# Performance work log

Measured on AMD Instinct MI355X. Metric: run time of the kernel, lower is better.

Reference implementation:

```python
import jax, jax.numpy as jnp
import numpy as np

EMBED_DIM = 400          # d; entity embedding is 2d (alpha|beta)
N_ENTITY = 100000
N_RELATION = 500
HIDDEN = 1600
BATCH = 8192


def _reg(x):
    # Regularizer(base_add=1, min_val=0.05, max_val=1e9)
    return jnp.clip(x + 1.0, 0.05, 1e9)


def setup_inputs() -> dict:
    key = jax.random.key(0)
    ks = jax.random.split(key, 16)
    d = EMBED_DIM
    rng = (9.0 + 2.0) / d  # (gamma + epsilon) / embed_dim with gamma=9

    def xavier(k, shape):
        fan_out, fan_in = shape
        lim = np.sqrt(6.0 / (fan_in + fan_out))
        return jax.random.uniform(k, shape, jnp.float32, -lim, lim)

    inp = {
        "anchor1_idx": jax.random.randint(ks[0], (BATCH,), 0, N_ENTITY),
        "rel1_idx": jax.random.randint(ks[1], (BATCH,), 0, N_RELATION),
        "anchor2_idx": jax.random.randint(ks[2], (BATCH,), 0, N_ENTITY),
        "rel2_idx": jax.random.randint(ks[3], (BATCH,), 0, N_RELATION),
        # embedding tables
        "entity_embedding": jax.random.uniform(ks[4], (N_ENTITY, 2 * d), jnp.float32, -rng, rng),
        "relation_embedding": jax.random.uniform(ks[5], (N_RELATION, d), jnp.float32, -rng, rng),
        # BetaProjection: layer1 [hidden, 2d+d], layer2 [hidden, hidden], layer0 [2d, hidden]
        "pW1": xavier(ks[6], (HIDDEN, 3 * d)),
        "pb1": jnp.zeros((HIDDEN,), jnp.float32),
        "pW2": xavier(ks[7], (HIDDEN, HIDDEN)),
        "pb2": jnp.zeros((HIDDEN,), jnp.float32),
        "pW0": xavier(ks[8], (2 * d, HIDDEN)),
        "pb0": jnp.zeros((2 * d,), jnp.float32),
        # BetaIntersection: layer1 [2d, 2d], layer2 [d, 2d]
        "iW1": xavier(ks[9], (2 * d, 2 * d)),
        "ib1": jnp.zeros((2 * d,), jnp.float32),
        "iW2": xavier(ks[10], (d, 2 * d)),
        "ib2": jnp.zeros((d,), jnp.float32),
    }
    return inp


def _projection(e_emb, r_emb, pW1, pb1, pW2, pb2, pW0, pb0):
    # cat -> Linear+ReLU (layer1) -> Linear+ReLU (layer2) -> layer0 -> regularizer
    x = jnp.concatenate([e_emb, r_emb], axis=-1)           # [B, 3d]
    x = jax.nn.relu(x @ pW1.T + pb1)                       # [B, H]
    x = jax.nn.relu(x @ pW2.T + pb2)                       # [B, H]
    x = x @ pW0.T + pb0                                    # [B, 2d]
    return _reg(x)


def _intersection(alphas, betas, iW1, ib1, iW2, ib2):
    # alphas/betas: [K, B, d]; softmax attention over K
    all_emb = jnp.concatenate([alphas, betas], axis=-1)    # [K, B, 2d]
    h = jax.nn.relu(all_emb @ iW1.T + ib1)                 # [K, B, 2d]
    att = jax.nn.softmax(h @ iW2.T + ib2, axis=0)          # [K, B, d]
    return jnp.sum(att * alphas, axis=0), jnp.sum(att * betas, axis=0)


def reference(anchor1_idx, rel1_idx, anchor2_idx, rel2_idx,
              entity_embedding, relation_embedding,
              pW1, pb1, pW2, pb2, pW0, pb0,
              iW1, ib1, iW2, ib2):
    h = _reg(entity_embedding)                             # entity_regularizer
    r = relation_embedding

    emb1 = _projection(h[anchor1_idx], r[rel1_idx], pW1, pb1, pW2, pb2, pW0, pb0)
    a1, b1 = jnp.split(emb1, 2, axis=-1)
    emb2 = _projection(h[anchor2_idx], r[rel2_idx], pW1, pb1, pW2, pb2, pW0, pb0)
    a2, b2 = jnp.split(emb2, 2, axis=-1)

    alpha, beta = _intersection(jnp.stack([a1, a2]), jnp.stack([b1, b2]),
                                iW1, ib1, iW2, ib2)
    return alpha, beta
```

## Files before the change

### kernel.cpp

```cpp
#include <hip/hip_runtime.h>
#include <hip/hip_bf16.h>
#include <stdint.h>

typedef __bf16 bf16_t;
typedef __bf16 bf16x8 __attribute__((ext_vector_type(8)));
typedef float f32x4 __attribute__((ext_vector_type(4)));

constexpr int BATCH = 8192;
constexpr int M = 2 * BATCH;

constexpr int K1 = 1216;
constexpr int N1c = 1792;
constexpr int LDC1 = 1664, NS1 = 1600;
constexpr int LDA2 = 1664, KL2 = 1600;
constexpr int N2c = 1792;
constexpr int LDC2 = 1664, NS2 = 1600;
constexpr int LDA3 = 1664, KL3 = 1600;
constexpr int N3c = 1024;
constexpr int LDC3 = 1024, NS3 = 832;
constexpr int LDA4 = 1024, KL4 = 832;
constexpr int N4c = 1024;
constexpr int LDC4 = 1024, NS4 = 832;
constexpr int LDA5 = 1024, KL5 = 832, N5 = 512;

__device__ __forceinline__ void gload_lds16(const void* g, void* l) {
  __builtin_amdgcn_global_load_lds(
      (const __attribute__((address_space(1))) void*)g,
      (__attribute__((address_space(3))) void*)l,
      16, 0, 0);
}

#define CFENCE() asm volatile("" ::: "memory")
#define BAR()  { CFENCE(); __builtin_amdgcn_s_barrier(); CFENCE(); }

__device__ __forceinline__ void doconv(int idx, const float* __restrict__ src,
                                       bf16_t* __restrict__ dst, int Nr, int Kc, int Kp) {
  const int kp4 = Kp >> 2;
  const int r = idx / kp4;
  const int c = (idx - r * kp4) << 2;
  union { bf16_t h[4]; uint2 u; } pk;
#pragma unroll
  for (int j = 0; j < 4; ++j) {
    const int cc = c + j;
    const float v = (r < Nr && cc < Kc) ? src[(size_t)r * Kc + cc] : 0.f;
    pk.h[j] = (bf16_t)v;
  }
  *(uint2*)(dst + (size_t)r * Kp + c) = pk.u;
}

constexpr int CJ0 = N1c * K1 / 4;
constexpr int CJ1 = CJ0 + N2c * LDA2 / 4;
constexpr int CJ2 = CJ1 + N3c * LDA3 / 4;
constexpr int CJ3 = CJ2 + N4c * LDA4 / 4;
constexpr int CJ4 = CJ3 + N5 * LDA5 / 4;
constexpr int CONV_BLOCKS = CJ4 / 256;
constexpr int PREP_BLOCKS = M + CONV_BLOCKS;

__global__ void prep_kernel(const int* __restrict__ a1, const int* __restrict__ r1,
                            const int* __restrict__ a2, const int* __restrict__ r2,
                            const float* __restrict__ ent, const float* __restrict__ rel,
                            bf16_t* __restrict__ X,
                            const float* __restrict__ pW1, const float* __restrict__ pW2,
                            const float* __restrict__ pW0, const float* __restrict__ iW1,
                            const float* __restrict__ iW2,
                            bf16_t* __restrict__ W1b, bf16_t* __restrict__ W2b,
                            bf16_t* __restrict__ W0b, bf16_t* __restrict__ iW1b,
                            bf16_t* __restrict__ iW2b) {
  if (blockIdx.x < M) {
    const int row = blockIdx.x;
    const int b   = row & (BATCH - 1);
    const int br  = row >> 13;
    const int eidx = br ? a2[b] : a1[b];
    const int ridx = br ? r2[b] : r1[b];
    const float* __restrict__ esrc = ent + (size_t)eidx * 800;
    const float* __restrict__ rsrc = rel + (size_t)ridx * 400;
    bf16_t* __restrict__ dst = X + (size_t)row * K1;
    for (int g = threadIdx.x; g < K1 / 4; g += 256) {
      const int c = g * 4;
      float4 v = make_float4(0.f, 0.f, 0.f, 0.f);
      if (c < 800) {
        v = *(const float4*)(esrc + c);
        v.x = fminf(fmaxf(v.x + 1.f, 0.05f), 1e9f);
        v.y = fminf(fmaxf(v.y + 1.f, 0.05f), 1e9f);
        v.z = fminf(fmaxf(v.z + 1.f, 0.05f), 1e9f);
        v.w = fminf(fmaxf(v.w + 1.f, 0.05f), 1e9f);
      } else if (c < 1200) {
        v = *(const float4*)(rsrc + (c - 800));
      }
      union { bf16_t h[4]; uint2 u; } pk;
      pk.h[0] = (bf16_t)v.x; pk.h[1] = (bf16_t)v.y;
      pk.h[2] = (bf16_t)v.z; pk.h[3] = (bf16_t)v.w;
      *(uint2*)(dst + c) = pk.u;
    }
  } else {
    const int idx = (blockIdx.x - M) * 256 + threadIdx.x;
    if (idx < CJ0)      doconv(idx,        pW1, W1b, 1600, 1200, K1);
    else if (idx < CJ1) doconv(idx - CJ0,  pW2, W2b, 1600, 1600, LDA2);
    else if (idx < CJ2) doconv(idx - CJ1,  pW0, W0b,  800, 1600, LDA3);
    else if (idx < CJ3) doconv(idx - CJ2,  iW1, iW1b, 800,  800, LDA4);
    else if (idx < CJ4) doconv(idx - CJ3,  iW2, iW2b, 400,  800, LDA5);
  }
}

enum { ACT_RELU = 0, ACT_REG = 1 };

template <int ACT>
__global__ __launch_bounds__(512)
void gemm256(const bf16_t* __restrict__ A, const bf16_t* __restrict__ Bw,
             const float* __restrict__ bias, int Nbias,
             bf16_t* __restrict__ Cb,
             int lda, int Nstore, int ldc, int NT, int gridN) {
  __shared__ __align__(16) bf16_t lds[8][8192];

  const int nwg = gridDim.x;
  const int id = blockIdx.x;
  const int swz = (id & 7) * (nwg >> 3) + (id >> 3);
  const int bn = swz % gridN, bm = swz / gridN;

  const int t = threadIdx.x;
  const int lane = t & 63;
  const int wv = t >> 6;
  const int wm = wv >> 2, wn = wv & 3;
  const int l15 = lane & 15;
  const int kbs = (((lane >> 4) ^ ((l15 >> 1) & 3)) << 4);

  const int srow = t >> 2;
  const int skc  = (t & 3) ^ ((t >> 3) & 3);
  const bf16_t* aR0 = A  + (size_t)(bm * 256 + srow) * lda + skc * 8;
  const bf16_t* aR1 = aR0 + (size_t)128 * lda;
  const bf16_t* bR0 = Bw + (size_t)(bn * 256 + srow) * lda + skc * 8;
  const bf16_t* bR1 = bR0 + (size_t)128 * lda;
  const int ldsb0 = (wv * 64) * 16;
  const int ldsb1 = (512 + wv * 64) * 16;

  auto STAGE = [&](const bf16_t* r0p, const bf16_t* r1p, int kOff, bf16_t* slot) {
    gload_lds16(r0p + kOff, (char*)slot + ldsb0);
    gload_lds16(r1p + kOff, (char*)slot + ldsb1);
  };

  f32x4 acc[8][4];
#pragma unroll
  for (int i = 0; i < 8; ++i)
#pragma unroll
    for (int j = 0; j < 4; ++j) acc[i][j] = f32x4{0.f, 0.f, 0.f, 0.f};

  STAGE(aR0, aR1, 0, lds[0]);
  STAGE(bR0, bR1, 0, lds[2]);
  STAGE(aR0, aR1, 32, lds[1]);
  STAGE(bR0, bR1, 32, lds[3]);
  if (NT > 1) {
    STAGE(aR0, aR1, 64, lds[4]);
    STAGE(bR0, bR1, 64, lds[6]);
    asm volatile("s_waitcnt vmcnt(8)" ::: "memory");
  } else {
    asm volatile("s_waitcnt vmcnt(4)" ::: "memory");
  }
  __builtin_amdgcn_s_barrier();
  CFENCE();

  bf16x8 bfr[4];
  int db = 0;
  for (int kt = 0; kt < NT; ++kt, db ^= 1) {
    const bool p1 = (kt + 1) < NT;
    const bool p2 = (kt + 2) < NT;
    bf16_t* const cur = (bf16_t*)lds[db * 4];
    bf16_t* const nxt = (bf16_t*)lds[(db ^ 1) * 4];

    {
      const char* sA = (const char*)(cur);
      const char* sB = (const char*)(cur + 2 * 8192);
      bf16x8 af[4];
#pragma unroll
      for (int i = 0; i < 4; ++i)
        af[i] = *(const bf16x8*)(sA + ((wm * 128 + i * 16 + l15) << 6) + kbs);
#pragma unroll
      for (int i = 0; i < 4; ++i)
        bfr[i] = *(const bf16x8*)(sB + ((wn * 64 + i * 16 + l15) << 6) + kbs);
      if (p1) STAGE(aR0, aR1, (kt + 1) * 64 + 32, nxt + 1 * 8192);
      BAR();
      __builtin_amdgcn_s_setprio(1);
#pragma unroll
      for (int i = 0; i < 4; ++i)
#pragma unroll
        for (int j = 0; j < 4; ++j)
          acc[i][j] = __builtin_amdgcn_mfma_f32_16x16x32_bf16(af[i], bfr[j], acc[i][j], 0, 0, 0);
      __builtin_amdgcn_s_setprio(0);
      BAR();
    }
    {
      const char* sA = (const char*)(cur);
      bf16x8 af[4];
#pragma unroll
      for (int i = 0; i < 4; ++i)
        af[i] = *(const bf16x8*)(sA + ((wm * 128 + (4 + i) * 16 + l15) << 6) + kbs);
      if (p1) STAGE(bR0, bR1, (kt + 1) * 64 + 32, nxt + 3 * 8192);
      BAR();
      __builtin_amdgcn_s_setprio(1);
#pragma unroll
      for (int i = 0; i < 4; ++i)
#pragma unroll
        for (int j = 0; j < 4; ++j)
          acc[4 + i][j] = __builtin_amdgcn_mfma_f32_16x16x32_bf16(af[i], bfr[j], acc[4 + i][j], 0, 0, 0);
      __builtin_amdgcn_s_setprio(0);
      if (p1) asm volatile("s_waitcnt vmcnt(8)" ::: "memory");
      else    asm volatile("s_waitcnt vmcnt(0)" ::: "memory");
      BAR();
    }
    {
      const char* sA = (const char*)(cur + 1 * 8192);
      const char* sB = (const char*)(cur + 3 * 8192);
      bf16x8 af[4];
#pragma unroll
      for (int i = 0; i < 4; ++i)
        af[i] = *(const bf16x8*)(sA + ((wm * 128 + i * 16 + l15) << 6) + kbs);
#pragma unroll
      for (int i = 0; i < 4; ++i)
        bfr[i] = *(const bf16x8*)(sB + ((wn * 64 + i * 16 + l15) << 6) + kbs);
      if (p2) STAGE(aR0, aR1, (kt + 2) * 64, cur + 0 * 8192);
      BAR();
      __builtin_amdgcn_s_setprio(1);
#pragma unroll
      for (int i = 0; i < 4; ++i)
#pragma unroll
        for (int j = 0; j < 4; ++j)
          acc[i][j] = __builtin_amdgcn_mfma_f32_16x16x32_bf16(af[i], bfr[j], acc[i][j], 0, 0, 0);
      __builtin_amdgcn_s_setprio(0);
      BAR();
    }
    {
      const char* sA = (const char*)(cur + 1 * 8192);
      bf16x8 af[4];
#pragma unroll
      for (int i = 0; i < 4; ++i)
        af[i] = *(const bf16x8*)(sA + ((wm * 128 + (4 + i) * 16 + l15) << 6) + kbs);
      if (p2) STAGE(bR0, bR1, (kt + 2) * 64, cur + 2 * 8192);
      BAR();
      __builtin_amdgcn_s_setprio(1);
#pragma unroll
      for (int i = 0; i < 4; ++i)
#pragma unroll
        for (int j = 0; j < 4; ++j)
          acc[4 + i][j] = __builtin_amdgcn_mfma_f32_16x16x32_bf16(af[i], bfr[j], acc[4 + i][j], 0, 0, 0);
      __builtin_amdgcn_s_setprio(0);
      if (p1) {
        if (p2) asm volatile("s_waitcnt vmcnt(8)" ::: "memory");
        else    asm volatile("s_waitcnt vmcnt(4)" ::: "memory");
      }
      BAR();
    }
  }

  const int r0 = bm * 256 + wm * 128 + ((lane >> 4) * 4);
  const int c0 = bn * 256 + wn * 64 + l15;
#pragma unroll
  for (int ni = 0; ni < 4; ++ni) {
    const int col = c0 + ni * 16;
    const float bv = (col < Nbias) ? bias[col] : 0.f;
    const bool cok = (col < Nstore);
#pragma unroll
    for (int mi = 0; mi < 8; ++mi) {
#pragma unroll
      for (int j = 0; j < 4; ++j) {
        float v = acc[mi][ni][j] + bv;
        if (ACT == ACT_RELU) v = fmaxf(v, 0.f);
        else                 v = fminf(fmaxf(v + 1.f, 0.05f), 1e9f);
        if (cok) Cb[(size_t)(r0 + mi * 16 + j) * ldc + col] = (bf16_t)v;
      }
    }
  }
}

__global__ __launch_bounds__(256)
void g5_combine(const bf16_t* __restrict__ H, const bf16_t* __restrict__ Wb,
                const float* __restrict__ ib2, const bf16_t* __restrict__ E,
                float* __restrict__ out) {
  __shared__ __align__(16) bf16_t As1[128 * 64];
  __shared__ __align__(16) bf16_t As2[128 * 64];
  __shared__ __align__(16) bf16_t Bs[128 * 64];

  const int bn = blockIdx.x, bm = blockIdx.y;
  const int t = threadIdx.x;
  const int lane = t & 63;
  const int wv = t >> 6;
  const int wm = wv >> 1, wn = wv & 1;

  f32x4 acc1[4][4], acc2[4][4];
#pragma unroll
  for (int i = 0; i < 4; ++i)
#pragma unroll
    for (int j = 0; j < 4; ++j) { acc1[i][j] = f32x4{0.f,0.f,0.f,0.f}; acc2[i][j] = f32x4{0.f,0.f,0.f,0.f}; }

  const size_t a1Base = (size_t)(bm * 128) * LDA5;
  const size_t a2Base = (size_t)(8192 + bm * 128) * LDA5;
  const size_t bBase  = (size_t)(bn * 128) * LDA5;

  for (int kt = 0; kt < KL5; kt += 64) {
    __syncthreads();
#pragma unroll
    for (int q = 0; q < 4; ++q) {
      const int lin = q * 256 + t;
      const int row = lin >> 3;
      const int kc = ((lin & 7) ^ (row & 7)) * 8;
      const int lofs = (q * 256 + wv * 64) * 16;
      gload_lds16(H + a1Base + (size_t)row * LDA5 + kt + kc, (char*)As1 + lofs);
      gload_lds16(H + a2Base + (size_t)row * LDA5 + kt + kc, (char*)As2 + lofs);
      gload_lds16(Wb + bBase + (size_t)row * LDA5 + kt + kc, (char*)Bs + lofs);
    }
    __syncthreads();

#pragma unroll
    for (int s = 0; s < 2; ++s) {
      const int crd = s * 4 + (lane >> 4);
      const int k0 = (crd ^ (lane & 7)) * 8;
      bf16x8 af1[4], af2[4], bf[4];
#pragma unroll
      for (int i = 0; i < 4; ++i) {
        const int ra = wm * 64 + i * 16 + (lane & 15);
        af1[i] = *(const bf16x8*)(As1 + ra * 64 + k0);
        af2[i] = *(const bf16x8*)(As2 + ra * 64 + k0);
        const int rb = wn * 64 + i * 16 + (lane & 15);
        bf[i] = *(const bf16x8*)(Bs + rb * 64 + k0);
      }
#pragma unroll
      for (int mi = 0; mi < 4; ++mi)
#pragma unroll
        for (int ni = 0; ni < 4; ++ni) {
          acc1[mi][ni] = __builtin_amdgcn_mfma_f32_16x16x32_bf16(af1[mi], bf[ni], acc1[mi][ni], 0, 0, 0);
          acc2[mi][ni] = __builtin_amdgcn_mfma_f32_16x16x32_bf16(af2[mi], bf[ni], acc2[mi][ni], 0, 0, 0);
        }
    }
  }

  const int rloc0 = wm * 64 + ((lane >> 4) * 4);
  const int cloc0 = wn * 64 + (lane & 15);
#pragma unroll
  for (int ni = 0; ni < 4; ++ni) {
    const int d = bn * 128 + cloc0 + ni * 16;
    if (d >= 400) continue;
    const float bv = ib2[d];
#pragma unroll
    for (int mi = 0; mi < 4; ++mi) {
#pragma unroll
      for (int j = 0; j < 4; ++j) {
        const int b = bm * 128 + rloc0 + mi * 16 + j;
        const float l1 = acc1[mi][ni][j] + bv;
        const float l2 = acc2[mi][ni][j] + bv;
        const float att1 = 1.f / (1.f + expf(l2 - l1));
        const float att2 = 1.f - att1;
        const bf16_t* E1 = E + (size_t)b * LDC3;
        const bf16_t* E2 = E + (size_t)(8192 + b) * LDC3;
        out[(size_t)b * 400 + d] =
            att1 * (float)E1[d] + att2 * (float)E2[d];
        out[(size_t)8192 * 400 + (size_t)b * 400 + d] =
            att1 * (float)E1[400 + d] + att2 * (float)E2[400 + d];
      }
    }
  }
}

extern "C" void kernel_launch(void* const* d_in, const int* in_sizes, int n_in,
                              void* d_out, int out_size, void* d_ws, size_t ws_size,
                              hipStream_t stream) {
  const int* a1 = (const int*)d_in[0];
  const int* r1 = (const int*)d_in[1];
  const int* a2 = (const int*)d_in[2];
  const int* r2 = (const int*)d_in[3];
  const float* ent = (const float*)d_in[4];
  const float* rel = (const float*)d_in[5];
  const float* pW1 = (const float*)d_in[6];
  const float* pb1 = (const float*)d_in[7];
  const float* pW2 = (const float*)d_in[8];
  const float* pb2 = (const float*)d_in[9];
  const float* pW0 = (const float*)d_in[10];
  const float* pb0 = (const float*)d_in[11];
  const float* iW1 = (const float*)d_in[12];
  const float* ib1 = (const float*)d_in[13];
  const float* iW2 = (const float*)d_in[14];
  const float* ib2 = (const float*)d_in[15];

  char* ws = (char*)d_ws;
  size_t o = 0;
  auto take = [&](size_t bytes) { char* p = ws + o; o += (bytes + 255) & ~(size_t)255; return p; };
  bf16_t* W1b  = (bf16_t*)take((size_t)N1c * K1 * 2);
  bf16_t* W2b  = (bf16_t*)take((size_t)N2c * LDA2 * 2);
  bf16_t* W0b  = (bf16_t*)take((size_t)N3c * LDA3 * 2);
  bf16_t* iW1b = (bf16_t*)take((size_t)N4c * LDA4 * 2);
  bf16_t* iW2b = (bf16_t*)take((size_t)N5 * LDA5 * 2);
  char* bufX = take((size_t)M * K1 * 2);
  char* bufY = take((size_t)M * LDC1 * 2);
  char* bufZ = take((size_t)M * LDC2 * 2);

  bf16_t* Xb = (bf16_t*)bufX;
  bf16_t* Yb = (bf16_t*)bufY;
  bf16_t* Zb = (bf16_t*)bufZ;
  bf16_t* Eb = (bf16_t*)bufX;
  bf16_t* Hb = (bf16_t*)bufY;

  prep_kernel<<<dim3(PREP_BLOCKS), 256, 0, stream>>>(a1, r1, a2, r2, ent, rel, Xb,
                                                     pW1, pW2, pW0, iW1, iW2,
                                                     W1b, W2b, W0b, iW1b, iW2b);

  gemm256<ACT_RELU><<<dim3((N1c / 256) * (M / 256)), 512, 0, stream>>>(
      Xb, W1b, pb1, 1600, Yb, K1, NS1, LDC1, K1 / 64, N1c / 256);
  gemm256<ACT_RELU><<<dim3((N2c / 256) * (M / 256)), 512, 0, stream>>>(
      Yb, W2b, pb2, 1600, Zb, LDA2, NS2, LDC2, KL2 / 64, N2c / 256);
  gemm256<ACT_REG><<<dim3((N3c / 256) * (M / 256)), 512, 0, stream>>>(
      Zb, W0b, pb0, 800, Eb, LDA3, NS3, LDC3, KL3 / 64, N3c / 256);
  gemm256<ACT_RELU><<<dim3((N4c / 256) * (M / 256)), 512, 0, stream>>>(
      Eb, iW1b, ib1, 800, Hb, LDA4, NS4, LDC4, KL4 / 64, N4c / 256);
  g5_combine<<<dim3(N5 / 128, BATCH / 128), 256, 0, stream>>>(
      Hb, iW2b, ib2, Eb, (float*)d_out);
}
```

Measured before the change: 348.7 us.

## Use mixed 192/256-wide N tiles for hidden GEMMs, double-buffer g5, grid-stride prep

```diff
diff --git a/kernel.cpp b/kernel.cpp
--- a/kernel.cpp
+++ b/kernel.cpp
@@ -10,10 +10,8 @@
 constexpr int M = 2 * BATCH;
 
 constexpr int K1 = 1216;
-constexpr int N1c = 1792;
 constexpr int LDC1 = 1664, NS1 = 1600;
 constexpr int LDA2 = 1664, KL2 = 1600;
-constexpr int N2c = 1792;
 constexpr int LDC2 = 1664, NS2 = 1600;
 constexpr int LDA3 = 1664, KL3 = 1600;
 constexpr int N3c = 1024;
@@ -22,6 +20,7 @@
 constexpr int N4c = 1024;
 constexpr int LDC4 = 1024, NS4 = 832;
 constexpr int LDA5 = 1024, KL5 = 832, N5 = 512;
+constexpr int NW1 = 1792, NW2 = 1792;
 
 __device__ __forceinline__ void gload_lds16(const void* g, void* l) {
   __builtin_amdgcn_global_load_lds(
@@ -48,13 +47,14 @@
   *(uint2*)(dst + (size_t)r * Kp + c) = pk.u;
 }
 
-constexpr int CJ0 = N1c * K1 / 4;
-constexpr int CJ1 = CJ0 + N2c * LDA2 / 4;
+constexpr int CJ0 = NW1 * K1 / 4;
+constexpr int CJ1 = CJ0 + NW2 * LDA2 / 4;
 constexpr int CJ2 = CJ1 + N3c * LDA3 / 4;
 constexpr int CJ3 = CJ2 + N4c * LDA4 / 4;
 constexpr int CJ4 = CJ3 + N5 * LDA5 / 4;
-constexpr int CONV_BLOCKS = CJ4 / 256;
-constexpr int PREP_BLOCKS = M + CONV_BLOCKS;
+constexpr int GATHERB = 2048;
+constexpr int CONVB = 2048;
+constexpr int PREPB = GATHERB + CONVB;
 
 __global__ void prep_kernel(const int* __restrict__ a1, const int* __restrict__ r1,
                             const int* __restrict__ a2, const int* __restrict__ r2,
@@ -66,217 +66,238 @@
                             bf16_t* __restrict__ W1b, bf16_t* __restrict__ W2b,
                             bf16_t* __restrict__ W0b, bf16_t* __restrict__ iW1b,
                             bf16_t* __restrict__ iW2b) {
-  if (blockIdx.x < M) {
-    const int row = blockIdx.x;
-    const int b   = row & (BATCH - 1);
-    const int br  = row >> 13;
-    const int eidx = br ? a2[b] : a1[b];
-    const int ridx = br ? r2[b] : r1[b];
-    const float* __restrict__ esrc = ent + (size_t)eidx * 800;
-    const float* __restrict__ rsrc = rel + (size_t)ridx * 400;
-    bf16_t* __restrict__ dst = X + (size_t)row * K1;
-    for (int g = threadIdx.x; g < K1 / 4; g += 256) {
-      const int c = g * 4;
-      float4 v = make_float4(0.f, 0.f, 0.f, 0.f);
-      if (c < 800) {
-        v = *(const float4*)(esrc + c);
-        v.x = fminf(fmaxf(v.x + 1.f, 0.05f), 1e9f);
-        v.y = fminf(fmaxf(v.y + 1.f, 0.05f), 1e9f);
-        v.z = fminf(fmaxf(v.z + 1.f, 0.05f), 1e9f);
-        v.w = fminf(fmaxf(v.w + 1.f, 0.05f), 1e9f);
-      } else if (c < 1200) {
-        v = *(const float4*)(rsrc + (c - 800));
+  if (blockIdx.x < GATHERB) {
+    for (int r8 = 0; r8 < 8; ++r8) {
+      const int row = blockIdx.x * 8 + r8;
+      const int b   = row & (BATCH - 1);
+      const int br  = row >> 13;
+      const int eidx = br ? a2[b] : a1[b];
+      const int ridx = br ? r2[b] : r1[b];
+      const float* __restrict__ esrc = ent + (size_t)eidx * 800;
+      const float* __restrict__ rsrc = rel + (size_t)ridx * 400;
+      bf16_t* __restrict__ dst = X + (size_t)row * K1;
+      for (int g = threadIdx.x; g < K1 / 4; g += 256) {
+        const int c = g * 4;
+        float4 v = make_float4(0.f, 0.f, 0.f, 0.f);
+        if (c < 800) {
+          v = *(const float4*)(esrc + c);
+          v.x = fminf(fmaxf(v.x + 1.f, 0.05f), 1e9f);
+          v.y = fminf(fmaxf(v.y + 1.f, 0.05f), 1e9f);
+          v.z = fminf(fmaxf(v.z + 1.f, 0.05f), 1e9f);
+          v.w = fminf(fmaxf(v.w + 1.f, 0.05f), 1e9f);
+        } else if (c < 1200) {
+          v = *(const float4*)(rsrc + (c - 800));
+        }
+        union { bf16_t h[4]; uint2 u; } pk;
+        pk.h[0] = (bf16_t)v.x; pk.h[1] = (bf16_t)v.y;
+        pk.h[2] = (bf16_t)v.z; pk.h[3] = (bf16_t)v.w;
+        *(uint2*)(dst + c) = pk.u;
       }
-      union { bf16_t h[4]; uint2 u; } pk;
-      pk.h[0] = (bf16_t)v.x; pk.h[1] = (bf16_t)v.y;
-      pk.h[2] = (bf16_t)v.z; pk.h[3] = (bf16_t)v.w;
-      *(uint2*)(dst + c) = pk.u;
     }
   } else {
-    const int idx = (blockIdx.x - M) * 256 + threadIdx.x;
-    if (idx < CJ0)      doconv(idx,        pW1, W1b, 1600, 1200, K1);
-    else if (idx < CJ1) doconv(idx - CJ0,  pW2, W2b, 1600, 1600, LDA2);
-    else if (idx < CJ2) doconv(idx - CJ1,  pW0, W0b,  800, 1600, LDA3);
-    else if (idx < CJ3) doconv(idx - CJ2,  iW1, iW1b, 800,  800, LDA4);
-    else if (idx < CJ4) doconv(idx - CJ3,  iW2, iW2b, 400,  800, LDA5);
+    for (int idx = (blockIdx.x - GATHERB) * 256 + threadIdx.x; idx < CJ4;
+         idx += CONVB * 256) {
+      if (idx < CJ0)      doconv(idx,        pW1, W1b, 1600, 1200, K1);
+      else if (idx < CJ1) doconv(idx - CJ0,  pW2, W2b, 1600, 1600, LDA2);
+      else if (idx < CJ2) doconv(idx - CJ1,  pW0, W0b,  800, 1600, LDA3);
+      else if (idx < CJ3) doconv(idx - CJ2,  iW1, iW1b, 800,  800, LDA4);
+      else                doconv(idx - CJ3,  iW2, iW2b, 400,  800, LDA5);
+    }
   }
 }
 
 enum { ACT_RELU = 0, ACT_REG = 1 };
 
-template <int ACT>
+template <int ACT, int NFR>
+__device__ __forceinline__
+void gemm_body(const bf16_t* __restrict__ A, const bf16_t* __restrict__ Bw,
+               const float* __restrict__ bias, int Nbias, bf16_t* __restrict__ Cb,
+               int lda, int Nstore, int ldc, int NT, int bm, int col0,
+               bf16_t* ldsbase, int t) {
+  const int lane = t & 63;
+  const int wv = t >> 6;
+  const int wm = wv >> 2, wn = wv & 3;
+  const int l15 = lane & 15;
+  const int kbs = (((lane >> 4) ^ ((l15 >> 1) & 3)) << 4);
+
+  const int srow = t >> 2;
+  const int skc  = (t & 3) ^ ((t >> 3) & 3);
+  const bf16_t* aR0 = A  + (size_t)(bm * 256 + srow) * lda + skc * 8;
+  const bf16_t* aR1 = aR0 + (size_t)128 * lda;
+  const bf16_t* bR0 = Bw + (size_t)(col0 + srow) * lda + skc * 8;
+  const bf16_t* bR1 = bR0 + (size_t)128 * lda;
+  const int ldsb0 = (wv * 64) * 16;
+  const int ldsb1 = (512 + wv * 64) * 16;
+
+  auto SLOT = [&](int s) { return ldsbase + s * 8192; };
+  auto STAGE = [&](const bf16_t* r0p, const bf16_t* r1p, int kOff, bf16_t* slot) {
+    gload_lds16(r0p + kOff, (char*)slot + ldsb0);
+    gload_lds16(r1p + kOff, (char*)slot + ldsb1);
+  };
+
+  f32x4 acc[8][NFR];
+#pragma unroll
+  for (int i = 0; i < 8; ++i)
+#pragma unroll
+    for (int j = 0; j < NFR; ++j) acc[i][j] = f32x4{0.f, 0.f, 0.f, 0.f};
+
+  STAGE(aR0, aR1, 0, SLOT(0));
+  STAGE(bR0, bR1, 0, SLOT(2));
+  STAGE(aR0, aR1, 32, SLOT(1));
+  STAGE(bR0, bR1, 32, SLOT(3));
+  if (NT > 1) {
+    STAGE(aR0, aR1, 64, SLOT(4));
+    STAGE(bR0, bR1, 64, SLOT(6));
+    asm volatile("s_waitcnt vmcnt(8)" ::: "memory");
+  } else {
+    asm volatile("s_waitcnt vmcnt(4)" ::: "memory");
+  }
+  __builtin_amdgcn_s_barrier();
+  CFENCE();
+
+  bf16x8 bfr[NFR];
+  int db = 0;
+  for (int kt = 0; kt < NT; ++kt, db ^= 1) {
+    const bool p1 = (kt + 1) < NT;
+    const bool p2 = (kt + 2) < NT;
+    bf16_t* const cur = SLOT(db * 4);
+    bf16_t* const nxt = SLOT((db ^ 1) * 4);
+
+    {
+      const char* sA = (const char*)(cur);
+      const char* sB = (const char*)(cur + 2 * 8192);
+      bf16x8 af[4];
+#pragma unroll
+      for (int i = 0; i < 4; ++i)
+        af[i] = *(const bf16x8*)(sA + ((wm * 128 + i * 16 + l15) << 6) + kbs);
+#pragma unroll
+      for (int i = 0; i < NFR; ++i)
+        bfr[i] = *(const bf16x8*)(sB + ((wn * (NFR * 16) + i * 16 + l15) << 6) + kbs);
+      if (p1) STAGE(aR0, aR1, (kt + 1) * 64 + 32, nxt + 1 * 8192);
+      BAR();
+      __builtin_amdgcn_s_setprio(1);
+#pragma unroll
+      for (int i = 0; i < 4; ++i)
+#pragma unroll
+        for (int j = 0; j < NFR; ++j)
+          acc[i][j] = __builtin_amdgcn_mfma_f32_16x16x32_bf16(af[i], bfr[j], acc[i][j], 0, 0, 0);
+      __builtin_amdgcn_s_setprio(0);
+      BAR();
+    }
+    {
+      const char* sA = (const char*)(cur);
+      bf16x8 af[4];
+#pragma unroll
+      for (int i = 0; i < 4; ++i)
+        af[i] = *(const bf16x8*)(sA + ((wm * 128 + (4 + i) * 16 + l15) << 6) + kbs);
+      if (p1) STAGE(bR0, bR1, (kt + 1) * 64 + 32, nxt + 3 * 8192);
+      BAR();
+      __builtin_amdgcn_s_setprio(1);
+#pragma unroll
+      for (int i = 0; i < 4; ++i)
+#pragma unroll
+        for (int j = 0; j < NFR; ++j)
+          acc[4 + i][j] = __builtin_amdgcn_mfma_f32_16x16x32_bf16(af[i], bfr[j], acc[4 + i][j], 0, 0, 0);
+      __builtin_amdgcn_s_setprio(0);
+      if (p1) asm volatile("s_waitcnt vmcnt(8)" ::: "memory");
+      else    asm volatile("s_waitcnt vmcnt(0)" ::: "memory");
+      BAR();
+    }
+    {
+      const char* sA = (const char*)(cur + 1 * 8192);
+      const char* sB = (const char*)(cur + 3 * 8192);
+      bf16x8 af[4];
+#pragma unroll
+      for (int i = 0; i < 4; ++i)
+        af[i] = *(const bf16x8*)(sA + ((wm * 128 + i * 16 + l15) << 6) + kbs);
+#pragma unroll
+      for (int i = 0; i < NFR; ++i)
+        bfr[i] = *(const bf16x8*)(sB + ((wn * (NFR * 16) + i * 16 + l15) << 6) + kbs);
+      if (p2) STAGE(aR0, aR1, (kt + 2) * 64, cur + 0 * 8192);
+      BAR();
+      __builtin_amdgcn_s_setprio(1);
+#pragma unroll
+      for (int i = 0; i < 4; ++i)
+#pragma unroll
+        for (int j = 0; j < NFR; ++j)
+          acc[i][j] = __builtin_amdgcn_mfma_f32_16x16x32_bf16(af[i], bfr[j], acc[i][j], 0, 0, 0);
+      __builtin_amdgcn_s_setprio(0);
+      BAR();
+    }
+    {
+      const char* sA = (const char*)(cur + 1 * 8192);
+      bf16x8 af[4];
+#pragma unroll
+      for (int i = 0; i < 4; ++i)
+        af[i] = *(const bf16x8*)(sA + ((wm * 128 + (4 + i) * 16 + l15) << 6) + kbs);
+      if (p2) STAGE(bR0, bR1, (kt + 2) * 64, cur + 2 * 8192);
+      BAR();
+      __builtin_amdgcn_s_setprio(1);
+#pragma unroll
+      for (int i = 0; i < 4; ++i)
+#pragma unroll
+        for (int j = 0; j < NFR; ++j)
+          acc[4 + i][j] = __builtin_amdgcn_mfma_f32_16x16x32_bf16(af[i], bfr[j], acc[4 + i][j], 0, 0, 0);
+      __builtin_amdgcn_s_setprio(0);
+      if (p1) {
+        if (p2) asm volatile("s_waitcnt vmcnt(8)" ::: "memory");
+        else    asm volatile("s_waitcnt vmcnt(4)" ::: "memory");
+      }
+      BAR();
+    }
+  }
+
+  const int r0 = bm * 256 + wm * 128 + ((lane >> 4) * 4);
+  const int c0 = col0 + wn * (NFR * 16) + l15;
+#pragma unroll
+  for (int ni = 0; ni < NFR; ++ni) {
+    const int col = c0 + ni * 16;
+    const float bv = (col < Nbias) ? bias[col] : 0.f;
+    const bool cok = (col < Nstore);
+#pragma unroll
+    for (int mi = 0; mi < 8; ++mi) {
+#pragma unroll
+      for (int j = 0; j < 4; ++j) {
+        float v = acc[mi][ni][j] + bv;
+        if (ACT == ACT_RELU) v = fmaxf(v, 0.f);
+        else                 v = fminf(fmaxf(v + 1.f, 0.05f), 1e9f);
+        if (cok) Cb[(size_t)(r0 + mi * 16 + j) * ldc + col] = (bf16_t)v;
+      }
+    }
+  }
+}
+
+template <int ACT, bool MIXED>
 __global__ __launch_bounds__(512)
 void gemm256(const bf16_t* __restrict__ A, const bf16_t* __restrict__ Bw,
              const float* __restrict__ bias, int Nbias,
              bf16_t* __restrict__ Cb,
              int lda, int Nstore, int ldc, int NT, int gridN) {
   __shared__ __align__(16) bf16_t lds[8][8192];
-
   const int nwg = gridDim.x;
   const int id = blockIdx.x;
   const int swz = (id & 7) * (nwg >> 3) + (id >> 3);
   const int bn = swz % gridN, bm = swz / gridN;
-
   const int t = threadIdx.x;
-  const int lane = t & 63;
-  const int wv = t >> 6;
-  const int wm = wv >> 2, wn = wv & 3;
-  const int l15 = lane & 15;
-  const int kbs = (((lane >> 4) ^ ((l15 >> 1) & 3)) << 4);
-
-  const int srow = t >> 2;
-  const int skc  = (t & 3) ^ ((t >> 3) & 3);
-  const bf16_t* aR0 = A  + (size_t)(bm * 256 + srow) * lda + skc * 8;
-  const bf16_t* aR1 = aR0 + (size_t)128 * lda;
-  const bf16_t* bR0 = Bw + (size_t)(bn * 256 + srow) * lda + skc * 8;
-  const bf16_t* bR1 = bR0 + (size_t)128 * lda;
-  const int ldsb0 = (wv * 64) * 16;
-  const int ldsb1 = (512 + wv * 64) * 16;
-
-  auto STAGE = [&](const bf16_t* r0p, const bf16_t* r1p, int kOff, bf16_t* slot) {
-    gload_lds16(r0p + kOff, (char*)slot + ldsb0);
-    gload_lds16(r1p + kOff, (char*)slot + ldsb1);
-  };
-
-  f32x4 acc[8][4];
-#pragma unroll
-  for (int i = 0; i < 8; ++i)
-#pragma unroll
-    for (int j = 0; j < 4; ++j) acc[i][j] = f32x4{0.f, 0.f, 0.f, 0.f};
-
-  STAGE(aR0, aR1, 0, lds[0]);
-  STAGE(bR0, bR1, 0, lds[2]);
-  STAGE(aR0, aR1, 32, lds[1]);
-  STAGE(bR0, bR1, 32, lds[3]);
-  if (NT > 1) {
-    STAGE(aR0, aR1, 64, lds[4]);
-    STAGE(bR0, bR1, 64, lds[6]);
-    asm volatile("s_waitcnt vmcnt(8)" ::: "memory");
+  if (MIXED) {
+    const int col0 = bn * 192;
+    if (bn < gridN - 1)
+      gemm_body<ACT, 3>(A, Bw, bias, Nbias, Cb, lda, Nstore, ldc, NT, bm, col0, &lds[0][0], t);
+    else
+      gemm_body<ACT, 4>(A, Bw, bias, Nbias, Cb, lda, Nstore, ldc, NT, bm, col0, &lds[0][0], t);
   } else {
-    asm volatile("s_waitcnt vmcnt(4)" ::: "memory");
-  }
-  __builtin_amdgcn_s_barrier();
-  CFENCE();
-
-  bf16x8 bfr[4];
-  int db = 0;
-  for (int kt = 0; kt < NT; ++kt, db ^= 1) {
-    const bool p1 = (kt + 1) < NT;
-    const bool p2 = (kt + 2) < NT;
-    bf16_t* const cur = (bf16_t*)lds[db * 4];
-    bf16_t* const nxt = (bf16_t*)lds[(db ^ 1) * 4];
-
-    {
-      const char* sA = (const char*)(cur);
-      const char* sB = (const char*)(cur + 2 * 8192);
-      bf16x8 af[4];
-#pragma unroll
-      for (int i = 0; i < 4; ++i)
-        af[i] = *(const bf16x8*)(sA + ((wm * 128 + i * 16 + l15) << 6) + kbs);
-#pragma unroll
-      for (int i = 0; i < 4; ++i)
-        bfr[i] = *(const bf16x8*)(sB + ((wn * 64 + i * 16 + l15) << 6) + kbs);
-      if (p1) STAGE(aR0, aR1, (kt + 1) * 64 + 32, nxt + 1 * 8192);
-      BAR();
-      __builtin_amdgcn_s_setprio(1);
-#pragma unroll
-      for (int i = 0; i < 4; ++i)
-#pragma unroll
-        for (int j = 0; j < 4; ++j)
-          acc[i][j] = __builtin_amdgcn_mfma_f32_16x16x32_bf16(af[i], bfr[j], acc[i][j], 0, 0, 0);
-      __builtin_amdgcn_s_setprio(0);
-      BAR();
-    }
-    {
-      const char* sA = (const char*)(cur);
-      bf16x8 af[4];
-#pragma unroll
-      for (int i = 0; i < 4; ++i)
-        af[i] = *(const bf16x8*)(sA + ((wm * 128 + (4 + i) * 16 + l15) << 6) + kbs);
-      if (p1) STAGE(bR0, bR1, (kt + 1) * 64 + 32, nxt + 3 * 8192);
-      BAR();
-      __builtin_amdgcn_s_setprio(1);
-#pragma unroll
-      for (int i = 0; i < 4; ++i)
-#pragma unroll
-        for (int j = 0; j < 4; ++j)
-          acc[4 + i][j] = __builtin_amdgcn_mfma_f32_16x16x32_bf16(af[i], bfr[j], acc[4 + i][j], 0, 0, 0);
-      __builtin_amdgcn_s_setprio(0);
-      if (p1) asm volatile("s_waitcnt vmcnt(8)" ::: "memory");
-      else    asm volatile("s_waitcnt vmcnt(0)" ::: "memory");
-      BAR();
-    }
-    {
-      const char* sA = (const char*)(cur + 1 * 8192);
-      const char* sB = (const char*)(cur + 3 * 8192);
-      bf16x8 af[4];
-#pragma unroll
-      for (int i = 0; i < 4; ++i)
-        af[i] = *(const bf16x8*)(sA + ((wm * 128 + i * 16 + l15) << 6) + kbs);
-#pragma unroll
-      for (int i = 0; i < 4; ++i)
-        bfr[i] = *(const bf16x8*)(sB + ((wn * 64 + i * 16 + l15) << 6) + kbs);
-      if (p2) STAGE(aR0, aR1, (kt + 2) * 64, cur + 0 * 8192);
-      BAR();
-      __builtin_amdgcn_s_setprio(1);
-#pragma unroll
-      for (int i = 0; i < 4; ++i)
-#pragma unroll
-        for (int j = 0; j < 4; ++j)
-          acc[i][j] = __builtin_amdgcn_mfma_f32_16x16x32_bf16(af[i], bfr[j], acc[i][j], 0, 0, 0);
-      __builtin_amdgcn_s_setprio(0);
-      BAR();
-    }
-    {
-      const char* sA = (const char*)(cur + 1 * 8192);
-      bf16x8 af[4];
-#pragma unroll
-      for (int i = 0; i < 4; ++i)
-        af[i] = *(const bf16x8*)(sA + ((wm * 128 + (4 + i) * 16 + l15) << 6) + kbs);
-      if (p2) STAGE(bR0, bR1, (kt + 2) * 64, cur + 2 * 8192);
-      BAR();
-      __builtin_amdgcn_s_setprio(1);
-#pragma unroll
-      for (int i = 0; i < 4; ++i)
-#pragma unroll
-        for (int j = 0; j < 4; ++j)
-          acc[4 + i][j] = __builtin_amdgcn_mfma_f32_16x16x32_bf16(af[i], bfr[j], acc[4 + i][j], 0, 0, 0);
-      __builtin_amdgcn_s_setprio(0);
-      if (p1) {
-        if (p2) asm volatile("s_waitcnt vmcnt(8)" ::: "memory");
-        else    asm volatile("s_waitcnt vmcnt(4)" ::: "memory");
-      }
-      BAR();
-    }
-  }
-
-  const int r0 = bm * 256 + wm * 128 + ((lane >> 4) * 4);
-  const int c0 = bn * 256 + wn * 64 + l15;
-#pragma unroll
-  for (int ni = 0; ni < 4; ++ni) {
-    const int col = c0 + ni * 16;
-    const float bv = (col < Nbias) ? bias[col] : 0.f;
-    const bool cok = (col < Nstore);
-#pragma unroll
-    for (int mi = 0; mi < 8; ++mi) {
-#pragma unroll
-      for (int j = 0; j < 4; ++j) {
-        float v = acc[mi][ni][j] + bv;
-        if (ACT == ACT_RELU) v = fmaxf(v, 0.f);
-        else                 v = fminf(fmaxf(v + 1.f, 0.05f), 1e9f);
-        if (cok) Cb[(size_t)(r0 + mi * 16 + j) * ldc + col] = (bf16_t)v;
-      }
-    }
-  }
-}
-
+    gemm_body<ACT, 4>(A, Bw, bias, Nbias, Cb, lda, Nstore, ldc, NT, bm, bn * 256, &lds[0][0], t);
+  }
+}
+
+constexpr int NT5 = KL5 / 64;
 __global__ __launch_bounds__(256)
 void g5_combine(const bf16_t* __restrict__ H, const bf16_t* __restrict__ Wb,
                 const float* __restrict__ ib2, const bf16_t* __restrict__ E,
                 float* __restrict__ out) {
-  __shared__ __align__(16) bf16_t As1[128 * 64];
-  __shared__ __align__(16) bf16_t As2[128 * 64];
-  __shared__ __align__(16) bf16_t Bs[128 * 64];
+  __shared__ __align__(16) bf16_t As1[2][8192];
+  __shared__ __align__(16) bf16_t As2[2][8192];
+  __shared__ __align__(16) bf16_t Bs[2][8192];
 
   const int bn = blockIdx.x, bm = blockIdx.y;
   const int t = threadIdx.x;
@@ -294,20 +315,24 @@
   const size_t a2Base = (size_t)(8192 + bm * 128) * LDA5;
   const size_t bBase  = (size_t)(bn * 128) * LDA5;
 
-  for (int kt = 0; kt < KL5; kt += 64) {
-    __syncthreads();
+  auto stage = [&](int db, int kt) {
 #pragma unroll
     for (int q = 0; q < 4; ++q) {
       const int lin = q * 256 + t;
       const int row = lin >> 3;
       const int kc = ((lin & 7) ^ (row & 7)) * 8;
       const int lofs = (q * 256 + wv * 64) * 16;
-      gload_lds16(H + a1Base + (size_t)row * LDA5 + kt + kc, (char*)As1 + lofs);
-      gload_lds16(H + a2Base + (size_t)row * LDA5 + kt + kc, (char*)As2 + lofs);
-      gload_lds16(Wb + bBase + (size_t)row * LDA5 + kt + kc, (char*)Bs + lofs);
-    }
-    __syncthreads();
-
+      gload_lds16(H + a1Base + (size_t)row * LDA5 + kt + kc, (char*)As1[db] + lofs);
+      gload_lds16(H + a2Base + (size_t)row * LDA5 + kt + kc, (char*)As2[db] + lofs);
+      gload_lds16(Wb + bBase + (size_t)row * LDA5 + kt + kc, (char*)Bs[db] + lofs);
+    }
+  };
+
+  stage(0, 0);
+  __syncthreads();
+  int db = 0;
+  for (int it = 0; it < NT5; ++it) {
+    if (it + 1 < NT5) stage(db ^ 1, (it + 1) * 64);
 #pragma unroll
     for (int s = 0; s < 2; ++s) {
       const int crd = s * 4 + (lane >> 4);
@@ -316,10 +341,10 @@
 #pragma unroll
       for (int i = 0; i < 4; ++i) {
         const int ra = wm * 64 + i * 16 + (lane & 15);
-        af1[i] = *(const bf16x8*)(As1 + ra * 64 + k0);
-        af2[i] = *(const bf16x8*)(As2 + ra * 64 + k0);
+        af1[i] = *(const bf16x8*)(As1[db] + ra * 64 + k0);
+        af2[i] = *(const bf16x8*)(As2[db] + ra * 64 + k0);
         const int rb = wn * 64 + i * 16 + (lane & 15);
-        bf[i] = *(const bf16x8*)(Bs + rb * 64 + k0);
+        bf[i] = *(const bf16x8*)(Bs[db] + rb * 64 + k0);
       }
 #pragma unroll
       for (int mi = 0; mi < 4; ++mi)
@@ -329,6 +354,8 @@
           acc2[mi][ni] = __builtin_amdgcn_mfma_f32_16x16x32_bf16(af2[mi], bf[ni], acc2[mi][ni], 0, 0, 0);
         }
     }
+    __syncthreads();
+    db ^= 1;
   }
 
   const int rloc0 = wm * 64 + ((lane >> 4) * 4);
@@ -381,8 +408,8 @@
   char* ws = (char*)d_ws;
   size_t o = 0;
   auto take = [&](size_t bytes) { char* p = ws + o; o += (bytes + 255) & ~(size_t)255; return p; };
-  bf16_t* W1b  = (bf16_t*)take((size_t)N1c * K1 * 2);
-  bf16_t* W2b  = (bf16_t*)take((size_t)N2c * LDA2 * 2);
+  bf16_t* W1b  = (bf16_t*)take((size_t)NW1 * K1 * 2);
+  bf16_t* W2b  = (bf16_t*)take((size_t)NW2 * LDA2 * 2);
   bf16_t* W0b  = (bf16_t*)take((size_t)N3c * LDA3 * 2);
   bf16_t* iW1b = (bf16_t*)take((size_t)N4c * LDA4 * 2);
   bf16_t* iW2b = (bf16_t*)take((size_t)N5 * LDA5 * 2);
@@ -396,18 +423,18 @@
   bf16_t* Eb = (bf16_t*)bufX;
   bf16_t* Hb = (bf16_t*)bufY;
 
-  prep_kernel<<<dim3(PREP_BLOCKS), 256, 0, stream>>>(a1, r1, a2, r2, ent, rel, Xb,
-                                                     pW1, pW2, pW0, iW1, iW2,
-                                                     W1b, W2b, W0b, iW1b, iW2b);
-
-  gemm256<ACT_RELU><<<dim3((N1c / 256) * (M / 256)), 512, 0, stream>>>(
-      Xb, W1b, pb1, 1600, Yb, K1, NS1, LDC1, K1 / 64, N1c / 256);
-  gemm256<ACT_RELU><<<dim3((N2c / 256) * (M / 256)), 512, 0, stream>>>(
-      Yb, W2b, pb2, 1600, Zb, LDA2, NS2, LDC2, KL2 / 64, N2c / 256);
-  gemm256<ACT_REG><<<dim3((N3c / 256) * (M / 256)), 512, 0, stream>>>(
-      Zb, W0b, pb0, 800, Eb, LDA3, NS3, LDC3, KL3 / 64, N3c / 256);
-  gemm256<ACT_RELU><<<dim3((N4c / 256) * (M / 256)), 512, 0, stream>>>(
-      Eb, iW1b, ib1, 800, Hb, LDA4, NS4, LDC4, KL4 / 64, N4c / 256);
+  prep_kernel<<<dim3(PREPB), 256, 0, stream>>>(a1, r1, a2, r2, ent, rel, Xb,
+                                               pW1, pW2, pW0, iW1, iW2,
+                                               W1b, W2b, W0b, iW1b, iW2b);
+
+  gemm256<ACT_RELU, true><<<dim3(8 * (M / 256)), 512, 0, stream>>>(
+      Xb, W1b, pb1, 1600, Yb, K1, NS1, LDC1, K1 / 64, 8);
+  gemm256<ACT_RELU, true><<<dim3(8 * (M / 256)), 512, 0, stream>>>(
+      Yb, W2b, pb2, 1600, Zb, LDA2, NS2, LDC2, KL2 / 64, 8);
+  gemm256<ACT_REG, false><<<dim3(4 * (M / 256)), 512, 0, stream>>>(
+      Zb, W0b, pb0, 800, Eb, LDA3, NS3, LDC3, KL3 / 64, 4);
+  gemm256<ACT_RELU, false><<<dim3(4 * (M / 256)), 512, 0, stream>>>(
+      Eb, iW1b, ib1, 800, Hb, LDA4, NS4, LDC4, KL4 / 64, 4);
   g5_combine<<<dim3(N5 / 128, BATCH / 128), 256, 0, stream>>>(
       Hb, iW2b, ib2, Eb, (float*)d_out);
 }
```

After: 349.0 us. About the same (+0.1%).
